# Optimization experiments

Hardware: AMD Instinct MI355X
Metric: run time of the kernel (lower is better)

Reference implementation:

```python
import jax, jax.numpy as jnp
import numpy as np

ROPE_THETA = 10000.0


def _rotate_half(x):
    # interleaved rotation: out[..., 2i] = -x[..., 2i+1], out[..., 2i+1] = x[..., 2i]
    x_even = x[..., ::2]
    x_odd = x[..., 1::2]
    return jnp.stack([-x_odd, x_even], axis=-1).reshape(x.shape)


def _rope_cos_sin(N, D, dtype):
    inv_freq = 1.0 / (ROPE_THETA ** (jnp.arange(0, D, 2, dtype=jnp.float32) / D))  # [D/2]
    angles = jnp.arange(N, dtype=jnp.float32)[:, None] * inv_freq[None, :]          # [N, D/2]
    angles = jnp.repeat(angles, 2, axis=-1)                                          # [N, D]
    cos = jnp.cos(angles).astype(dtype)[None, :, None, :]  # [1, N, 1, D]
    sin = jnp.sin(angles).astype(dtype)[None, :, None, :]
    return cos, sin


def setup_inputs() -> dict:
    key = jax.random.key(0)
    kq, kk, kv, km = jax.random.split(key, 4)
    B, N, H, D = 16, 1024, 8, 64
    xq = jax.random.normal(kq, (B, N, H, D), dtype=jnp.float32)
    xk = jax.random.normal(kk, (B, N, H, D), dtype=jnp.float32)
    xv = jax.random.normal(kv, (B, N, H, D), dtype=jnp.float32)
    vis_mask = jax.random.bernoulli(km, 0.8, (B, N))  # bool visibility mask per batch
    return {"xq": xq, "xk": xk, "xv": xv, "vis_mask": vis_mask}


def reference(xq, xk, xv, vis_mask):
    B, N, H, D = xq.shape
    sm_scale = 1.0 / np.sqrt(D).astype(np.float32)

    # RoPE (interleaved) on q and k
    cos, sin = _rope_cos_sin(N, D, xq.dtype)
    q = xq * cos + _rotate_half(xq) * sin
    k = xk * cos + _rotate_half(xk) * sin

    # masked full attention: scores [B, H, N, N]
    scores = jnp.einsum("bnhd,bmhd->bhnm", q, k) * sm_scale
    attn_mask = (vis_mask[:, None, :, None] & vis_mask[:, None, None, :])  # [B,1,N,N]
    scores = jnp.where(attn_mask, scores, -jnp.inf)
    p = jax.nn.softmax(scores, axis=-1)
    p = jnp.nan_to_num(p, nan=0.0)  # fully-masked rows -> zeros (matches fallback)
    out = jnp.einsum("bhnm,bmhd->bnhd", p, xv)
    return out
```

## Files before the change

### kernel.cpp

```cpp
#include <hip/hip_runtime.h>
#include <stdint.h>

#define Bb 16
#define Nn 1024
#define Hh 8
#define Dd 64

typedef unsigned short u16;
typedef float f32x4 __attribute__((ext_vector_type(4)));
typedef short short8 __attribute__((ext_vector_type(8)));

union U4S8 { uint4 u; short8 s; };

__device__ __forceinline__ uint32_t f2bf(float f){
  union{float f;uint32_t i;} v; v.f=f;
  return (v.i + 0x7fffu + ((v.i>>16)&1u))>>16;
}

__device__ __forceinline__ f32x4 mfma16(short8 a, short8 b, f32x4 c){
  return __builtin_amdgcn_mfma_f32_16x16x32_bf16(a,b,c,0,0,0);
}

#define ROPE_K 0.41524101186092030f

__global__ __launch_bounds__(256) void prepass_kernel(
    const float* __restrict__ xk, const float* __restrict__ xv,
    u16* __restrict__ Kr, u16* __restrict__ Vt)
{
  const int tid = threadIdx.x;
  const int bid = blockIdx.x;
  const int nt = bid & 15, h = (bid>>4)&7, b = bid>>7;
  const size_t bh = (size_t)b*Hh + h;

  {
    int r = tid>>2, c = (tid&3)<<4;
    int n = (nt<<6) + r;
    const float4* g = (const float4*)(xk + ((((size_t)b*Nn + n)*Hh + h)<<6) + c);
    float4 a0=g[0],a1=g[1],a2=g[2],a3=g[3];
    float xx[16] = {a0.x,a0.y,a0.z,a0.w, a1.x,a1.y,a1.z,a1.w,
                    a2.x,a2.y,a2.z,a2.w, a3.x,a3.y,a3.z,a3.w};
    uint32_t w[8];
    #pragma unroll
    for (int j=0;j<8;++j){
      int i = (c>>1)+j;
      float inv = exp2f(-(float)i * ROPE_K);
      float ang = (float)n * inv;
      float sn, cs; sincosf(ang, &sn, &cs);
      float x0 = xx[2*j], x1 = xx[2*j+1];
      float q0 = x0*cs - x1*sn;
      float q1 = x1*cs + x0*sn;
      w[j] = f2bf(q0) | (f2bf(q1)<<16);
    }
    u16* dst = Kr + ((bh<<10) + n - ((size_t)0))*0;
    dst = Kr + (((bh<<10) + (size_t)n)<<6) + c;
    *(uint4*)dst     = make_uint4(w[0],w[1],w[2],w[3]);
    *(uint4*)(dst+8) = make_uint4(w[4],w[5],w[6],w[7]);
  }

  {
    int k = tid&63, dstrip = (tid>>6)<<4;
    int n = (nt<<6) + k;
    const float4* g = (const float4*)(xv + ((((size_t)b*Nn + n)*Hh + h)<<6) + dstrip);
    float4 a0=g[0],a1=g[1],a2=g[2],a3=g[3];
    float vv[16] = {a0.x,a0.y,a0.z,a0.w, a1.x,a1.y,a1.z,a1.w,
                    a2.x,a2.y,a2.z,a2.w, a3.x,a3.y,a3.z,a3.w};
    #pragma unroll
    for (int j=0;j<16;++j)
      Vt[ ((bh<<6) + (size_t)(dstrip+j))*Nn + n ] = (u16)f2bf(vv[j]);
  }
}

__global__ __launch_bounds__(256,3) void attn2_kernel(
    const float* __restrict__ xq, const u16* __restrict__ Kr,
    const u16* __restrict__ Vt, const int* __restrict__ vis,
    float* __restrict__ out)
{
  __shared__ u16 Ks[64][72];
  __shared__ u16 Vs[64][72];
  __shared__ u16 Ps[4][32][64];

  const int tid  = threadIdx.x;
  const int wave = tid >> 6;
  const int lane = tid & 63;
  const int l15  = lane & 15;
  const int quad = lane >> 4;

  const int bid = blockIdx.x;
  const int qt = bid & 7;
  const int h  = (bid >> 3) & 7;
  const int b  = bid >> 6;
  const size_t bh = (size_t)b*Hh + h;

  short8 qa[2][2];
  #pragma unroll
  for (int mb=0; mb<2; ++mb){
    int n = (qt<<7) + (wave<<5) + (mb<<4) + l15;
    const float* src = xq + ((((size_t)b*Nn + n)*Hh + h)<<6);
    #pragma unroll
    for (int half=0; half<2; ++half){
      int d0 = (quad<<3) + (half<<5);
      const float4* g = (const float4*)(src + d0);
      float4 u0 = g[0], u1 = g[1];
      float xx[8] = {u0.x,u0.y,u0.z,u0.w, u1.x,u1.y,u1.z,u1.w};
      uint32_t w[4];
      #pragma unroll
      for (int j=0;j<4;++j){
        int i = (d0>>1) + j;
        float inv = exp2f(-(float)i * ROPE_K);
        float ang = (float)n * inv;
        float sn, cs; sincosf(ang, &sn, &cs);
        float x0 = xx[2*j], x1 = xx[2*j+1];
        float q0 = (x0*cs - x1*sn)*0.125f;
        float q1 = (x1*cs + x0*sn)*0.125f;
        w[j] = f2bf(q0) | (f2bf(q1)<<16);
      }
      U4S8 t; t.u = make_uint4(w[0],w[1],w[2],w[3]);
      qa[mb][half] = t.s;
    }
  }

  f32x4 acc[2][4];
  float l_r[2][4];
  #pragma unroll
  for (int mb=0;mb<2;++mb){
    #pragma unroll
    for (int s=0;s<4;++s) acc[mb][s] = (f32x4){0.f,0.f,0.f,0.f};
    #pragma unroll
    for (int rr=0;rr<4;++rr) l_r[mb][rr] = 0.f;
  }

  const u16* Krb = Kr + (bh<<16);
  const u16* Vtb = Vt + (bh<<16);
  const int* visb = vis + b*Nn;

  const int r = tid>>2, c16 = (tid&3)<<4;
  const int sw = l15>>2;

  for (int kt=0; kt<16; ++kt){
    __syncthreads();
    {
      const u16* ksrc = Krb + ((size_t)((kt<<6)+r)<<6) + c16;
      uint4 k0 = *(const uint4*)ksrc, k1 = *(const uint4*)(ksrc+8);
      const u16* vsrc = Vtb + ((size_t)r<<10) + (kt<<6) + c16;
      uint4 v0 = *(const uint4*)vsrc, v1 = *(const uint4*)(vsrc+8);
      *(uint4*)&Ks[r][c16]   = k0; *(uint4*)&Ks[r][c16+8] = k1;
      *(uint4*)&Vs[r][c16]   = v0; *(uint4*)&Vs[r][c16+8] = v1;
    }
    __syncthreads();

    f32x4 s4[2][4];
    #pragma unroll
    for (int n=0;n<4;++n){
      short8 kb0 = *(const short8*)&Ks[(n<<4)+l15][quad<<3];
      short8 kb1 = *(const short8*)&Ks[(n<<4)+l15][(quad<<3)+32];
      #pragma unroll
      for (int mb=0;mb<2;++mb){
        f32x4 t = (f32x4){0.f,0.f,0.f,0.f};
        t = mfma16(qa[mb][0], kb0, t);
        t = mfma16(qa[mb][1], kb1, t);
        s4[mb][n] = t;
      }
    }

    float vf[4];
    #pragma unroll
    for (int n=0;n<4;++n)
      vf[n] = (visb[(kt<<6)+(n<<4)+l15] != 0) ? 1.f : 0.f;

    #pragma unroll
    for (int mb=0;mb<2;++mb){
      #pragma unroll
      for (int n=0;n<4;++n){
        int coln = ((n ^ quad)<<4) + l15;
        #pragma unroll
        for (int rr=0;rr<4;++rr){
          float p = __expf(s4[mb][n][rr]) * vf[n];
          l_r[mb][rr] += p;
          Ps[wave][(mb<<4)+(quad<<2)+rr][coln] = (u16)f2bf(p);
        }
      }
    }
    asm volatile("s_waitcnt lgkmcnt(0)" ::: "memory");

    short8 pa[2][2];
    #pragma unroll
    for (int mb=0;mb<2;++mb){
      pa[mb][0] = *(const short8*)&Ps[wave][(mb<<4)+l15]
                    [ ((((quad>>1)  ) ^ sw)<<4) + ((quad&1)<<3) ];
      pa[mb][1] = *(const short8*)&Ps[wave][(mb<<4)+l15]
                    [ ((((quad>>1)+2) ^ sw)<<4) + ((quad&1)<<3) ];
    }

    #pragma unroll
    for (int s=0;s<4;++s){
      short8 vb0 = *(const short8*)&Vs[(s<<4)+l15][quad<<3];
      short8 vb1 = *(const short8*)&Vs[(s<<4)+l15][(quad<<3)+32];
      #pragma unroll
      for (int mb=0;mb<2;++mb){
        acc[mb][s] = mfma16(pa[mb][0], vb0, acc[mb][s]);
        acc[mb][s] = mfma16(pa[mb][1], vb1, acc[mb][s]);
      }
    }
  }

  #pragma unroll
  for (int mb=0;mb<2;++mb){
    #pragma unroll
    for (int rr=0;rr<4;++rr){
      float t = l_r[mb][rr];
      t += __shfl_xor(t,1); t += __shfl_xor(t,2);
      t += __shfl_xor(t,4); t += __shfl_xor(t,8);
      int qrow = (qt<<7) + (wave<<5) + (mb<<4) + (quad<<2) + rr;
      int qv = visb[qrow];
      float invl = (qv != 0 && t > 0.f) ? 1.f/t : 0.f;
      float* obase = out + ((((size_t)b*Nn + qrow)*Hh + h)<<6);
      #pragma unroll
      for (int s=0;s<4;++s)
        obase[(s<<4)+l15] = acc[mb][s][rr]*invl;
    }
  }
}

__device__ __forceinline__ void stage_rope_row_fb(const float* __restrict__ src,
                                                  u16 (*dst)[72],
                                                  int n_global, int sr, int d0)
{
  const float4* g = (const float4*)src;
  float4 a0 = g[0], a1 = g[1], a2 = g[2], a3 = g[3];
  float xx[16] = {a0.x,a0.y,a0.z,a0.w, a1.x,a1.y,a1.z,a1.w,
                  a2.x,a2.y,a2.z,a2.w, a3.x,a3.y,a3.z,a3.w};
  uint32_t w[8];
  #pragma unroll
  for (int j=0;j<8;++j){
    int i = (d0>>1)+j;
    float inv = exp2f(-(float)i * ROPE_K);
    float ang = (float)n_global * inv;
    float sn, cs; sincosf(ang, &sn, &cs);
    float x0 = xx[2*j], x1 = xx[2*j+1];
    float q0 = x0*cs - x1*sn;
    float q1 = x1*cs + x0*sn;
    w[j] = f2bf(q0) | (f2bf(q1)<<16);
  }
  *(uint4*)&dst[sr][d0]   = make_uint4(w[0],w[1],w[2],w[3]);
  *(uint4*)&dst[sr][d0+8] = make_uint4(w[4],w[5],w[6],w[7]);
}

__global__ __launch_bounds__(256,2) void attn_fallback(
    const float* __restrict__ xq, const float* __restrict__ xk,
    const float* __restrict__ xv, const int* __restrict__ vis,
    float* __restrict__ out)
{
  __shared__ u16 Qs[64][72];
  __shared__ u16 Ks[64][72];
  __shared__ u16 Vt[64][72];
  __shared__ u16 Ps[4][16][72];
  __shared__ float viss[64];

  const int tid  = threadIdx.x;
  const int wave = tid >> 6;
  const int lane = tid & 63;
  const int l15  = lane & 15;
  const int quad = lane >> 4;

  const int bid = blockIdx.x;
  const int qt = bid & 15;
  const int h  = (bid >> 4) & 7;
  const int b  = bid >> 7;

  const int sr = tid >> 2;
  const int d0 = (tid & 3) << 4;

  {
    int ng = (qt<<6) + sr;
    const float* src = xq + ((((size_t)b*Nn + ng)*Hh + h)<<6) + d0;
    stage_rope_row_fb(src, Qs, ng, sr, d0);
  }
  __syncthreads();

  short8 qa0 = *(const short8*)&Qs[(wave<<4)+l15][quad<<3];
  short8 qa1 = *(const short8*)&Qs[(wave<<4)+l15][(quad<<3)+32];

  f32x4 acc[4];
  #pragma unroll
  for (int s=0;s<4;++s) acc[s] = (f32x4){0.f,0.f,0.f,0.f};
  float m_r[4], l_r[4];
  #pragma unroll
  for (int rr=0;rr<4;++rr){ m_r[rr] = -1e30f; l_r[rr] = 0.f; }

  for (int kt=0; kt<16; ++kt){
    __syncthreads();
    {
      int ng = (kt<<6) + sr;
      const float* src = xk + ((((size_t)b*Nn + ng)*Hh + h)<<6) + d0;
      stage_rope_row_fb(src, Ks, ng, sr, d0);
    }
    {
      int ng = (kt<<6) + sr;
      const float4* g = (const float4*)(xv + ((((size_t)b*Nn + ng)*Hh + h)<<6) + d0);
      float4 a0 = g[0], a1 = g[1], a2 = g[2], a3 = g[3];
      float vv16[16] = {a0.x,a0.y,a0.z,a0.w, a1.x,a1.y,a1.z,a1.w,
                        a2.x,a2.y,a2.z,a2.w, a3.x,a3.y,a3.z,a3.w};
      #pragma unroll
      for (int j=0;j<16;++j) Vt[d0+j][sr] = (u16)f2bf(vv16[j]);
    }
    if (tid < 64) viss[tid] = (vis[b*Nn + (kt<<6) + tid] != 0) ? 1.f : 0.f;
    __syncthreads();

    f32x4 s4[4];
    #pragma unroll
    for (int n=0;n<4;++n){
      short8 kb0 = *(const short8*)&Ks[(n<<4)+l15][quad<<3];
      short8 kb1 = *(const short8*)&Ks[(n<<4)+l15][(quad<<3)+32];
      f32x4 t = (f32x4){0.f,0.f,0.f,0.f};
      t = mfma16(qa0, kb0, t);
      t = mfma16(qa1, kb1, t);
      s4[n] = t;
    }
    float vv[4];
    #pragma unroll
    for (int n=0;n<4;++n) vv[n] = viss[(n<<4)+l15];

    float p[4][4];
    #pragma unroll
    for (int rr=0; rr<4; ++rr){
      float sc[4];
      #pragma unroll
      for (int n=0;n<4;++n) sc[n] = (vv[n] > 0.f) ? s4[n][rr]*0.125f : -1e30f;
      float tm = fmaxf(fmaxf(sc[0],sc[1]), fmaxf(sc[2],sc[3]));
      tm = fmaxf(tm, __shfl_xor(tm,1));
      tm = fmaxf(tm, __shfl_xor(tm,2));
      tm = fmaxf(tm, __shfl_xor(tm,4));
      tm = fmaxf(tm, __shfl_xor(tm,8));
      float mnew  = fmaxf(m_r[rr], tm);
      float alpha = __expf(m_r[rr] - mnew);
      m_r[rr] = mnew;
      float psum = 0.f;
      #pragma unroll
      for (int n=0;n<4;++n){
        float pv = (vv[n] > 0.f) ? __expf(sc[n] - mnew) : 0.f;
        p[n][rr] = pv; psum += pv;
      }
      l_r[rr] = l_r[rr]*alpha + psum;
      #pragma unroll
      for (int s=0;s<4;++s) acc[s][rr] *= alpha;
    }

    #pragma unroll
    for (int n=0;n<4;++n)
      #pragma unroll
      for (int rr=0;rr<4;++rr)
        Ps[wave][(quad<<2)+rr][(n<<4)+l15] = (u16)f2bf(p[n][rr]);
    asm volatile("s_waitcnt lgkmcnt(0)" ::: "memory");
    short8 pa0 = *(const short8*)&Ps[wave][l15][quad<<3];
    short8 pa1 = *(const short8*)&Ps[wave][l15][(quad<<3)+32];

    #pragma unroll
    for (int s=0;s<4;++s){
      short8 vb0 = *(const short8*)&Vt[(s<<4)+l15][quad<<3];
      short8 vb1 = *(const short8*)&Vt[(s<<4)+l15][(quad<<3)+32];
      acc[s] = mfma16(pa0, vb0, acc[s]);
      acc[s] = mfma16(pa1, vb1, acc[s]);
    }
  }

  #pragma unroll
  for (int rr=0;rr<4;++rr){
    float t = l_r[rr];
    t += __shfl_xor(t,1); t += __shfl_xor(t,2);
    t += __shfl_xor(t,4); t += __shfl_xor(t,8);
    int row = (qt<<6) + (wave<<4) + (quad<<2) + rr;
    int qv  = vis[b*Nn + row];
    float invl = (qv != 0 && t > 0.f) ? 1.f/t : 0.f;
    size_t obase = (((size_t)b*Nn + row)*Hh + h) << 6;
    #pragma unroll
    for (int s=0;s<4;++s)
      out[obase + (s<<4) + l15] = acc[s][rr]*invl;
  }
}

extern "C" void kernel_launch(void* const* d_in, const int* in_sizes, int n_in,
                              void* d_out, int out_size, void* d_ws, size_t ws_size,
                              hipStream_t stream)
{
  const float* xq = (const float*)d_in[0];
  const float* xk = (const float*)d_in[1];
  const float* xv = (const float*)d_in[2];
  const int* vis  = (const int*)d_in[3];
  float* out = (float*)d_out;

  const size_t kv_elems = (size_t)Bb*Hh*Nn*Dd;
  const size_t need = 2*kv_elems*sizeof(u16);

  if (d_ws != nullptr && ws_size >= need){
    u16* Kr = (u16*)d_ws;
    u16* Vt = Kr + kv_elems;
    prepass_kernel<<<dim3(Bb*Hh*(Nn/64)), dim3(256), 0, stream>>>(xk, xv, Kr, Vt);
    attn2_kernel<<<dim3(Bb*Hh*(Nn/128)), dim3(256), 0, stream>>>(xq, Kr, Vt, vis, out);
  } else {
    attn_fallback<<<dim3(Bb*Hh*(Nn/64)), dim3(256), 0, stream>>>(xq, xk, xv, vis, out);
  }
}
```

Before: 195.8 us.

## Keep P in registers via transposed QK MFMA and permuted V layout

The score MFMA is computed as K·Q^T so each lane's accumulator outputs already form the A-operand fragment for the PV MFMA, once V is stored with a matching permuted key order in the prepass. This removes the per-tile LDS round trip for P. Softmax switches to exp2 with log2(e) folded into the Q scale, and the mask is read as int4. Each block now covers 256 query rows with 4 m-blocks per wave at occupancy 2, and a precomputed RoPE cos/sin table replaces per-element sincos. The cost is higher register pressure and an extra small kernel launch.

```diff
diff --git a/kernel.cpp b/kernel.cpp
--- a/kernel.cpp
+++ b/kernel.cpp
@@ -1,4 +1,5 @@
 #include <hip/hip_runtime.h>
+#include <hip/hip_bf16.h>
 #include <stdint.h>
 
 #define Bb 16
@@ -11,6 +12,7 @@
 typedef short short8 __attribute__((ext_vector_type(8)));
 
 union U4S8 { uint4 u; short8 s; };
+union BF2U { __hip_bfloat162 h; uint32_t u; };
 
 __device__ __forceinline__ uint32_t f2bf(float f){
   union{float f;uint32_t i;} v; v.f=f;
@@ -22,10 +24,21 @@
 }
 
 #define ROPE_K 0.41524101186092030f
+#define QS 0.18033688011112042f
+
+__global__ void rope_table_kernel(float2* __restrict__ tab){
+  int id = blockIdx.x*256 + threadIdx.x;
+  int n = id >> 5, i = id & 31;
+  float inv = exp2f(-(float)i * ROPE_K);
+  float a = (float)n * inv;
+  float s, c; sincosf(a, &s, &c);
+  tab[id] = make_float2(c, s);
+}
 
 __global__ __launch_bounds__(256) void prepass_kernel(
     const float* __restrict__ xk, const float* __restrict__ xv,
-    u16* __restrict__ Kr, u16* __restrict__ Vt)
+    const float2* __restrict__ tab,
+    u16* __restrict__ Kr, u16* __restrict__ Vp)
 {
   const int tid = threadIdx.x;
   const int bid = blockIdx.x;
@@ -43,41 +56,40 @@
     #pragma unroll
     for (int j=0;j<8;++j){
       int i = (c>>1)+j;
-      float inv = exp2f(-(float)i * ROPE_K);
-      float ang = (float)n * inv;
-      float sn, cs; sincosf(ang, &sn, &cs);
+      float cs, sn;
+      if (tab){ float2 t = tab[(n<<5)+i]; cs = t.x; sn = t.y; }
+      else { float inv = exp2f(-(float)i * ROPE_K); sincosf((float)n*inv, &sn, &cs); }
       float x0 = xx[2*j], x1 = xx[2*j+1];
       float q0 = x0*cs - x1*sn;
       float q1 = x1*cs + x0*sn;
       w[j] = f2bf(q0) | (f2bf(q1)<<16);
     }
-    u16* dst = Kr + ((bh<<10) + n - ((size_t)0))*0;
-    dst = Kr + (((bh<<10) + (size_t)n)<<6) + c;
+    u16* dst = Kr + (((bh<<10) + (size_t)n)<<6) + c;
     *(uint4*)dst     = make_uint4(w[0],w[1],w[2],w[3]);
     *(uint4*)(dst+8) = make_uint4(w[4],w[5],w[6],w[7]);
   }
 
   {
-    int k = tid&63, dstrip = (tid>>6)<<4;
+    int k = tid&63, ds = (tid>>6)<<4;
     int n = (nt<<6) + k;
-    const float4* g = (const float4*)(xv + ((((size_t)b*Nn + n)*Hh + h)<<6) + dstrip);
+    int slot = (k&1) | (((k>>4)&3)<<1) | (((k>>2)&3)<<3) | (((k>>1)&1)<<5);
+    const float4* g = (const float4*)(xv + ((((size_t)b*Nn + n)*Hh + h)<<6) + ds);
     float4 a0=g[0],a1=g[1],a2=g[2],a3=g[3];
     float vv[16] = {a0.x,a0.y,a0.z,a0.w, a1.x,a1.y,a1.z,a1.w,
                     a2.x,a2.y,a2.z,a2.w, a3.x,a3.y,a3.z,a3.w};
     #pragma unroll
     for (int j=0;j<16;++j)
-      Vt[ ((bh<<6) + (size_t)(dstrip+j))*Nn + n ] = (u16)f2bf(vv[j]);
-  }
-}
-
-__global__ __launch_bounds__(256,3) void attn2_kernel(
+      Vp[ (bh<<16) + ((size_t)(ds+j)<<10) + (nt<<6) + slot ] = (u16)f2bf(vv[j]);
+  }
+}
+
+__global__ __launch_bounds__(256,2) void attn3_kernel(
     const float* __restrict__ xq, const u16* __restrict__ Kr,
-    const u16* __restrict__ Vt, const int* __restrict__ vis,
-    float* __restrict__ out)
+    const u16* __restrict__ Vp, const int* __restrict__ vis,
+    const float2* __restrict__ tab, float* __restrict__ out)
 {
   __shared__ u16 Ks[64][72];
   __shared__ u16 Vs[64][72];
-  __shared__ u16 Ps[4][32][64];
 
   const int tid  = threadIdx.x;
   const int wave = tid >> 6;
@@ -86,19 +98,22 @@
   const int quad = lane >> 4;
 
   const int bid = blockIdx.x;
-  const int qt = bid & 7;
-  const int h  = (bid >> 3) & 7;
-  const int b  = bid >> 6;
+  const int qt = bid & 3;
+  const int h  = (bid >> 2) & 7;
+  const int b  = bid >> 5;
   const size_t bh = (size_t)b*Hh + h;
-
-  short8 qa[2][2];
-  #pragma unroll
-  for (int mb=0; mb<2; ++mb){
-    int n = (qt<<7) + (wave<<5) + (mb<<4) + l15;
+  const int qbase = qt<<8;
+
+  const int* visb = vis + b*Nn;
+
+  short8 qa[4][2];
+  #pragma unroll
+  for (int mb=0; mb<4; ++mb){
+    int n = qbase + (wave<<6) + (mb<<4) + l15;
     const float* src = xq + ((((size_t)b*Nn + n)*Hh + h)<<6);
     #pragma unroll
     for (int half=0; half<2; ++half){
-      int d0 = (quad<<3) + (half<<5);
+      int d0 = (half<<5) + (quad<<3);
       const float4* g = (const float4*)(src + d0);
       float4 u0 = g[0], u1 = g[1];
       float xx[8] = {u0.x,u0.y,u0.z,u0.w, u1.x,u1.y,u1.z,u1.w};
@@ -106,12 +121,12 @@
       #pragma unroll
       for (int j=0;j<4;++j){
         int i = (d0>>1) + j;
-        float inv = exp2f(-(float)i * ROPE_K);
-        float ang = (float)n * inv;
-        float sn, cs; sincosf(ang, &sn, &cs);
+        float cs, sn;
+        if (tab){ float2 t = tab[(n<<5)+i]; cs = t.x; sn = t.y; }
+        else { float inv = exp2f(-(float)i * ROPE_K); sincosf((float)n*inv, &sn, &cs); }
         float x0 = xx[2*j], x1 = xx[2*j+1];
-        float q0 = (x0*cs - x1*sn)*0.125f;
-        float q1 = (x1*cs + x0*sn)*0.125f;
+        float q0 = (x0*cs - x1*sn)*QS;
+        float q1 = (x1*cs + x0*sn)*QS;
         w[j] = f2bf(q0) | (f2bf(q1)<<16);
       }
       U4S8 t; t.u = make_uint4(w[0],w[1],w[2],w[3]);
@@ -119,76 +134,64 @@
     }
   }
 
-  f32x4 acc[2][4];
-  float l_r[2][4];
-  #pragma unroll
-  for (int mb=0;mb<2;++mb){
+  f32x4 acc[4][4];
+  float l_r[4];
+  #pragma unroll
+  for (int mb=0;mb<4;++mb){
+    l_r[mb] = 0.f;
     #pragma unroll
     for (int s=0;s<4;++s) acc[mb][s] = (f32x4){0.f,0.f,0.f,0.f};
-    #pragma unroll
-    for (int rr=0;rr<4;++rr) l_r[mb][rr] = 0.f;
   }
 
   const u16* Krb = Kr + (bh<<16);
-  const u16* Vtb = Vt + (bh<<16);
-  const int* visb = vis + b*Nn;
-
+  const u16* Vpb = Vp + (bh<<16);
   const int r = tid>>2, c16 = (tid&3)<<4;
-  const int sw = l15>>2;
 
   for (int kt=0; kt<16; ++kt){
     __syncthreads();
     {
       const u16* ksrc = Krb + ((size_t)((kt<<6)+r)<<6) + c16;
       uint4 k0 = *(const uint4*)ksrc, k1 = *(const uint4*)(ksrc+8);
-      const u16* vsrc = Vtb + ((size_t)r<<10) + (kt<<6) + c16;
+      const u16* vsrc = Vpb + ((size_t)r<<10) + (kt<<6) + c16;
       uint4 v0 = *(const uint4*)vsrc, v1 = *(const uint4*)(vsrc+8);
       *(uint4*)&Ks[r][c16]   = k0; *(uint4*)&Ks[r][c16+8] = k1;
       *(uint4*)&Vs[r][c16]   = v0; *(uint4*)&Vs[r][c16+8] = v1;
     }
     __syncthreads();
 
-    f32x4 s4[2][4];
-    #pragma unroll
-    for (int n=0;n<4;++n){
-      short8 kb0 = *(const short8*)&Ks[(n<<4)+l15][quad<<3];
-      short8 kb1 = *(const short8*)&Ks[(n<<4)+l15][(quad<<3)+32];
-      #pragma unroll
-      for (int mb=0;mb<2;++mb){
+    uint32_t pk[4][2][4];
+    #pragma unroll
+    for (int kb=0;kb<4;++kb){
+      short8 kf0 = *(const short8*)&Ks[(kb<<4)+l15][quad<<3];
+      short8 kf1 = *(const short8*)&Ks[(kb<<4)+l15][(quad<<3)+32];
+      int4 vi = *(const int4*)&visb[(kt<<6)+(kb<<4)+(quad<<2)];
+      float vf0 = vi.x ? 1.f : 0.f;
+      float vf1 = vi.y ? 1.f : 0.f;
+      float vf2 = vi.z ? 1.f : 0.f;
+      float vf3 = vi.w ? 1.f : 0.f;
+      #pragma unroll
+      for (int mb=0;mb<4;++mb){
         f32x4 t = (f32x4){0.f,0.f,0.f,0.f};
-        t = mfma16(qa[mb][0], kb0, t);
-        t = mfma16(qa[mb][1], kb1, t);
-        s4[mb][n] = t;
+        t = mfma16(kf0, qa[mb][0], t);
+        t = mfma16(kf1, qa[mb][1], t);
+        float p0 = exp2f(t.x)*vf0;
+        float p1 = exp2f(t.y)*vf1;
+        float p2 = exp2f(t.z)*vf2;
+        float p3 = exp2f(t.w)*vf3;
+        l_r[mb] += (p0+p1)+(p2+p3);
+        BF2U e0; e0.h = __float22bfloat162_rn(make_float2(p0,p1));
+        BF2U e1; e1.h = __float22bfloat162_rn(make_float2(p2,p3));
+        pk[kb][0][mb] = e0.u;
+        pk[kb][1][mb] = e1.u;
       }
     }
 
-    float vf[4];
-    #pragma unroll
-    for (int n=0;n<4;++n)
-      vf[n] = (visb[(kt<<6)+(n<<4)+l15] != 0) ? 1.f : 0.f;
-
-    #pragma unroll
-    for (int mb=0;mb<2;++mb){
-      #pragma unroll
-      for (int n=0;n<4;++n){
-        int coln = ((n ^ quad)<<4) + l15;
-        #pragma unroll
-        for (int rr=0;rr<4;++rr){
-          float p = __expf(s4[mb][n][rr]) * vf[n];
-          l_r[mb][rr] += p;
-          Ps[wave][(mb<<4)+(quad<<2)+rr][coln] = (u16)f2bf(p);
-        }
-      }
-    }
-    asm volatile("s_waitcnt lgkmcnt(0)" ::: "memory");
-
-    short8 pa[2][2];
-    #pragma unroll
-    for (int mb=0;mb<2;++mb){
-      pa[mb][0] = *(const short8*)&Ps[wave][(mb<<4)+l15]
-                    [ ((((quad>>1)  ) ^ sw)<<4) + ((quad&1)<<3) ];
-      pa[mb][1] = *(const short8*)&Ps[wave][(mb<<4)+l15]
-                    [ ((((quad>>1)+2) ^ sw)<<4) + ((quad&1)<<3) ];
+    short8 pa[4][2];
+    #pragma unroll
+    for (int mb=0;mb<4;++mb){
+      U4S8 a0; a0.u = make_uint4(pk[0][0][mb], pk[1][0][mb], pk[2][0][mb], pk[3][0][mb]);
+      U4S8 a1; a1.u = make_uint4(pk[0][1][mb], pk[1][1][mb], pk[2][1][mb], pk[3][1][mb]);
+      pa[mb][0] = a0.s; pa[mb][1] = a1.s;
     }
 
     #pragma unroll
@@ -196,7 +199,7 @@
       short8 vb0 = *(const short8*)&Vs[(s<<4)+l15][quad<<3];
       short8 vb1 = *(const short8*)&Vs[(s<<4)+l15][(quad<<3)+32];
       #pragma unroll
-      for (int mb=0;mb<2;++mb){
+      for (int mb=0;mb<4;++mb){
         acc[mb][s] = mfma16(pa[mb][0], vb0, acc[mb][s]);
         acc[mb][s] = mfma16(pa[mb][1], vb1, acc[mb][s]);
       }
@@ -204,19 +207,21 @@
   }
 
   #pragma unroll
-  for (int mb=0;mb<2;++mb){
+  for (int mb=0;mb<4;++mb){
+    float lv = l_r[mb];
+    lv += __shfl_xor(lv, 16);
+    lv += __shfl_xor(lv, 32);
+    int4 qvi = *(const int4*)&visb[qbase + (wave<<6) + (mb<<4) + (quad<<2)];
+    int qv[4] = {qvi.x, qvi.y, qvi.z, qvi.w};
     #pragma unroll
     for (int rr=0;rr<4;++rr){
-      float t = l_r[mb][rr];
-      t += __shfl_xor(t,1); t += __shfl_xor(t,2);
-      t += __shfl_xor(t,4); t += __shfl_xor(t,8);
-      int qrow = (qt<<7) + (wave<<5) + (mb<<4) + (quad<<2) + rr;
-      int qv = visb[qrow];
-      float invl = (qv != 0 && t > 0.f) ? 1.f/t : 0.f;
-      float* obase = out + ((((size_t)b*Nn + qrow)*Hh + h)<<6);
+      float lq = __shfl(lv, (quad<<2)+rr);
+      float invl = (qv[rr] != 0 && lq > 0.f) ? 1.f/lq : 0.f;
+      int qrow = qbase + (wave<<6) + (mb<<4) + (quad<<2) + rr;
+      float* ob = out + ((((size_t)b*Nn + qrow)*Hh + h)<<6);
       #pragma unroll
       for (int s=0;s<4;++s)
-        obase[(s<<4)+l15] = acc[mb][s][rr]*invl;
+        ob[(s<<4)+l15] = acc[mb][s][rr]*invl;
     }
   }
 }
@@ -389,13 +394,23 @@
   float* out = (float*)d_out;
 
   const size_t kv_elems = (size_t)Bb*Hh*Nn*Dd;
-  const size_t need = 2*kv_elems*sizeof(u16);
-
-  if (d_ws != nullptr && ws_size >= need){
+  const size_t kv_bytes = kv_elems*sizeof(u16);
+  const size_t tab_bytes = (size_t)Nn*32*sizeof(float2);
+  const size_t need_tab = tab_bytes + 2*kv_bytes;
+  const size_t need_kv  = 2*kv_bytes;
+
+  if (d_ws != nullptr && ws_size >= need_tab){
+    float2* tab = (float2*)d_ws;
+    u16* Kr = (u16*)((char*)d_ws + tab_bytes);
+    u16* Vp = Kr + kv_elems;
+    rope_table_kernel<<<dim3((Nn*32)/256), dim3(256), 0, stream>>>(tab);
+    prepass_kernel<<<dim3(Bb*Hh*(Nn/64)), dim3(256), 0, stream>>>(xk, xv, tab, Kr, Vp);
+    attn3_kernel<<<dim3(Bb*Hh*(Nn/256)), dim3(256), 0, stream>>>(xq, Kr, Vp, vis, tab, out);
+  } else if (d_ws != nullptr && ws_size >= need_kv){
     u16* Kr = (u16*)d_ws;
-    u16* Vt = Kr + kv_elems;
-    prepass_kernel<<<dim3(Bb*Hh*(Nn/64)), dim3(256), 0, stream>>>(xk, xv, Kr, Vt);
-    attn2_kernel<<<dim3(Bb*Hh*(Nn/128)), dim3(256), 0, stream>>>(xq, Kr, Vt, vis, out);
+    u16* Vp = Kr + kv_elems;
+    prepass_kernel<<<dim3(Bb*Hh*(Nn/64)), dim3(256), 0, stream>>>(xk, xv, nullptr, Kr, Vp);
+    attn3_kernel<<<dim3(Bb*Hh*(Nn/256)), dim3(256), 0, stream>>>(xq, Kr, Vp, vis, nullptr, out);
   } else {
     attn_fallback<<<dim3(Bb*Hh*(Nn/64)), dim3(256), 0, stream>>>(xq, xk, xv, vis, out);
   }
```

Result: slower. 206.2 us (+5.3%).
